# Kernel tuning notes

Measured on AMD Instinct MI355X. Metric: run time of the kernel, lower is better.

Reference implementation:

```python
import jax, jax.numpy as jnp
import numpy as np

LN_EPS = 1e-5


def setup_inputs() -> dict:
    key = jax.random.key(0)
    k0, k1, k2, k3 = jax.random.split(key, 4)
    b, X, Y, w1, w2, d = 16, 16, 16, 8, 8, 128
    heads = 4
    x = jax.random.normal(k0, (b, X, Y, w1, w2, d), dtype=jnp.float32)
    gamma = jnp.ones((d,), dtype=jnp.float32)
    beta = jnp.zeros((d,), dtype=jnp.float32)
    w_qkv = jax.random.normal(k1, (d, 3 * d), dtype=jnp.float32) * 0.02
    w_out = jax.random.normal(k2, (d, d), dtype=jnp.float32) * 0.02
    bias_table = jax.random.normal(k3, ((2 * w1 - 1) * (2 * w2 - 1), heads), dtype=jnp.float32) * 0.02
    return {"x": x, "gamma": gamma, "beta": beta, "w_qkv": w_qkv,
            "w_out": w_out, "bias_table": bias_table,
            "window_height": 8, "window_width": 8}


def _rel_pos_indices(wh, ww):
    gh = jnp.arange(wh)
    gw = jnp.arange(ww)
    grid = jnp.stack(jnp.meshgrid(gh, gw, indexing='ij'), axis=-1).reshape(-1, 2)  # [n, 2]
    rel = grid[:, None, :] - grid[None, :, :]  # [n, n, 2]
    rel = rel + jnp.array([wh - 1, ww - 1])
    return rel[..., 0] * (2 * ww - 1) + rel[..., 1]  # [n, n]


def reference(x, gamma, beta, w_qkv, w_out, bias_table, window_height, window_width):
    b, X, Y, w1, w2, d = x.shape
    heads = bias_table.shape[-1]
    dh = d // heads
    scale = dh ** -0.5

    # LayerNorm over channel dim
    mu = x.mean(axis=-1, keepdims=True)
    var = jnp.mean((x - mu) ** 2, axis=-1, keepdims=True)
    xn = (x - mu) * jax.lax.rsqrt(var + LN_EPS) * gamma + beta

    n = w1 * w2
    xn = xn.reshape(b * X * Y, n, d)  # [B, n, d], B = b*X*Y windows

    qkv = xn @ w_qkv  # [B, n, 3d]
    q, k, v = jnp.split(qkv, 3, axis=-1)
    def split_heads(t):
        return t.reshape(t.shape[0], n, heads, dh).transpose(0, 2, 1, 3)  # [B, h, n, dh]
    q, k, v = map(split_heads, (q, k, v))

    sim = jnp.einsum('bhid,bhjd->bhij', q * scale, k)  # [B, h, n, n]

    idx = _rel_pos_indices(window_height, window_width)  # [n, n]
    bias = bias_table[idx].transpose(2, 0, 1)  # [h, n, n]

    attn = jax.nn.softmax(sim + bias, axis=-1)
    out = jnp.einsum('bhij,bhjd->bhid', attn, v)  # [B, h, n, dh]
    out = out.transpose(0, 2, 1, 3).reshape(b * X * Y, w1, w2, d)
    out = out @ w_out
    return out.reshape(b, X, Y, w1, w2, d)
```

## Files before the change

### kernel.cpp

```cpp
#include <hip/hip_runtime.h>

typedef __attribute__((ext_vector_type(4))) short short4v;
typedef __attribute__((ext_vector_type(8))) short short8;
typedef __attribute__((ext_vector_type(4))) float f32x4;

#define NWIN 4096

__device__ __forceinline__ short f2bf(float f) {
    unsigned int u = __builtin_bit_cast(unsigned int, f);
    u += 0x7fffu + ((u >> 16) & 1u);
    return (short)(u >> 16);
}

__device__ __forceinline__ unsigned pack2h(float a, float b) {
    unsigned ua = __builtin_bit_cast(unsigned, a) + 0x8000u;
    unsigned ub = __builtin_bit_cast(unsigned, b) + 0x8000u;
    return (ua >> 16) | (ub & 0xffff0000u);
}

__device__ __forceinline__ short4v pk4h(float a, float b, float c, float d) {
    uint2 u;
    u.x = pack2h(a, b);
    u.y = pack2h(c, d);
    return __builtin_bit_cast(short4v, u);
}

#define LOG2E 1.4426950408889634f
#define QSCALE 0.17677669529663687f

__global__ void prep_kernel(const float* __restrict__ w_qkv,
                            const float* __restrict__ w_out,
                            const float* __restrict__ bias_table,
                            short* __restrict__ wqkvT,
                            short* __restrict__ woutT,
                            float* __restrict__ biasP)
{
    int id = blockIdx.x * 256 + threadIdx.x;
    if (id < 49152) {
        int j = id >> 7, k = id & 127;
        float v = w_qkv[k * 384 + j];
        if (j < 128) v *= (QSCALE * LOG2E);
        wqkvT[id] = f2bf(v);
    } else if (id < 65536) {
        int t = id - 49152;
        int j = t >> 7, k = t & 127;
        woutT[t] = f2bf(w_out[k * 128 + j]);
    } else if (id < 81920) {
        int t = id - 65536;
        int m  = t & 15;
        int ln = (t >> 4) & 63;
        int ib = (t >> 10) & 3;
        int h  = t >> 12;
        int lo = ln & 15, g = ln >> 4;
        int i = ib * 16 + lo;
        int j = (m >> 2) * 16 + g * 4 + (m & 3);
        int ri = i >> 3, ci = i & 7, rj = j >> 3, cj = j & 7;
        int idx = (ri - rj + 7) * 15 + (ci - cj + 7);
        biasP[t] = bias_table[idx * 4 + h] * LOG2E;
    }
}

__global__ __launch_bounds__(256, 3)
void attn_kernel(const float* __restrict__ x,
                 const float* __restrict__ gamma,
                 const float* __restrict__ beta,
                 const short* __restrict__ wqkvT,
                 const short* __restrict__ woutT,
                 const float* __restrict__ biasP,
                 float* __restrict__ out)
{
    __shared__ __align__(16) char smem[32768];

    const int tid = threadIdx.x;
    const int h  = tid >> 6;
    const int ln = tid & 63;
    const int lo = ln & 15, g = ln >> 4;

    const float* xwin = x + (size_t)blockIdx.x * 8192;

    float4 va[4][2];
    #pragma unroll
    for (int p = 0; p < 4; ++p) {
        int t = h * 16 + p * 4 + g;
        const float4* xr = (const float4*)(xwin + t * 128 + lo * 8);
        va[p][0] = xr[0];
        va[p][1] = xr[1];
    }

    short8 pwk[2];
    #pragma unroll
    for (int cb = 0; cb < 2; ++cb)
        pwk[cb] = *(const short8*)(wqkvT + (128 + h * 32 + cb * 16 + lo) * 128 + g * 8);

    float4 ga0 = ((const float4*)gamma)[lo * 2], ga1 = ((const float4*)gamma)[lo * 2 + 1];
    float4 be0 = ((const float4*)beta)[lo * 2],  be1 = ((const float4*)beta)[lo * 2 + 1];

    #pragma unroll
    for (int p = 0; p < 4; ++p) {
        int t = h * 16 + p * 4 + g;
        float4 v0 = va[p][0], v1 = va[p][1];
        float s  = v0.x + v0.y + v0.z + v0.w + v1.x + v1.y + v1.z + v1.w;
        float sq = v0.x*v0.x + v0.y*v0.y + v0.z*v0.z + v0.w*v0.w
                 + v1.x*v1.x + v1.y*v1.y + v1.z*v1.z + v1.w*v1.w;
        #pragma unroll
        for (int m = 1; m < 16; m <<= 1) {
            s  += __shfl_xor(s, m, 64);
            sq += __shfl_xor(sq, m, 64);
        }
        float mu  = s * (1.f / 128.f);
        float var = sq * (1.f / 128.f) - mu * mu;
        float rs  = rsqrtf(var + 1e-5f);
        float y0 = (v0.x - mu) * rs * ga0.x + be0.x;
        float y1 = (v0.y - mu) * rs * ga0.y + be0.y;
        float y2 = (v0.z - mu) * rs * ga0.z + be0.z;
        float y3 = (v0.w - mu) * rs * ga0.w + be0.w;
        float y4 = (v1.x - mu) * rs * ga1.x + be1.x;
        float y5 = (v1.y - mu) * rs * ga1.y + be1.y;
        float y6 = (v1.z - mu) * rs * ga1.z + be1.z;
        float y7 = (v1.w - mu) * rs * ga1.w + be1.w;
        uint4 pk;
        pk.x = pack2h(y0, y1); pk.y = pack2h(y2, y3);
        pk.z = pack2h(y4, y5); pk.w = pack2h(y6, y7);
        *(uint4*)(smem + ((t * 256 + lo * 16) ^ ((t & 7) << 4))) = pk;
    }
    __syncthreads();

    const f32x4 z4 = {0.f, 0.f, 0.f, 0.f};

    short4v kA[2][4], qB[2][4], vA[2][4];
    {
        f32x4 acc[2][4];
        #pragma unroll
        for (int a = 0; a < 2; ++a)
            #pragma unroll
            for (int b = 0; b < 4; ++b) acc[a][b] = z4;
        #pragma unroll
        for (int kk = 0; kk < 4; ++kk) {
            short8 xa[4];
            #pragma unroll
            for (int tb = 0; tb < 4; ++tb) {
                int t = tb * 16 + lo;
                xa[tb] = *(const short8*)(smem + ((t * 256 + kk * 64 + g * 16) ^ ((t & 7) << 4)));
            }
            #pragma unroll
            for (int cb = 0; cb < 2; ++cb) {
                short8 wkf = (kk == 0) ? pwk[cb]
                    : *(const short8*)(wqkvT + (128 + h * 32 + cb * 16 + lo) * 128 + kk * 32 + g * 8);
                #pragma unroll
                for (int tb = 0; tb < 4; ++tb)
                    acc[cb][tb] = __builtin_amdgcn_mfma_f32_16x16x32_bf16(wkf, xa[tb], acc[cb][tb], 0, 0, 0);
            }
        }
        #pragma unroll
        for (int ck = 0; ck < 2; ++ck)
            #pragma unroll
            for (int tb = 0; tb < 4; ++tb)
                kA[ck][tb] = pk4h(acc[ck][tb][0], acc[ck][tb][1], acc[ck][tb][2], acc[ck][tb][3]);
    }
    {
        f32x4 acc[2][4];
        #pragma unroll
        for (int a = 0; a < 2; ++a)
            #pragma unroll
            for (int b = 0; b < 4; ++b) acc[a][b] = z4;
        #pragma unroll
        for (int kk = 0; kk < 4; ++kk) {
            short8 xa[4];
            #pragma unroll
            for (int tb = 0; tb < 4; ++tb) {
                int t = tb * 16 + lo;
                xa[tb] = *(const short8*)(smem + ((t * 256 + kk * 64 + g * 16) ^ ((t & 7) << 4)));
            }
            #pragma unroll
            for (int cb = 0; cb < 2; ++cb) {
                short8 wqf = *(const short8*)(wqkvT + (h * 32 + cb * 16 + lo) * 128 + kk * 32 + g * 8);
                #pragma unroll
                for (int tb = 0; tb < 4; ++tb)
                    acc[cb][tb] = __builtin_amdgcn_mfma_f32_16x16x32_bf16(wqf, xa[tb], acc[cb][tb], 0, 0, 0);
            }
        }
        #pragma unroll
        for (int ck = 0; ck < 2; ++ck)
            #pragma unroll
            for (int tb = 0; tb < 4; ++tb)
                qB[ck][tb] = pk4h(acc[ck][tb][0], acc[ck][tb][1], acc[ck][tb][2], acc[ck][tb][3]);
    }
    {
        f32x4 acc[4][2];
        #pragma unroll
        for (int a = 0; a < 4; ++a)
            #pragma unroll
            for (int b = 0; b < 2; ++b) acc[a][b] = z4;
        #pragma unroll
        for (int kk = 0; kk < 4; ++kk) {
            short8 xa[4];
            #pragma unroll
            for (int tb = 0; tb < 4; ++tb) {
                int t = tb * 16 + lo;
                xa[tb] = *(const short8*)(smem + ((t * 256 + kk * 64 + g * 16) ^ ((t & 7) << 4)));
            }
            #pragma unroll
            for (int cb = 0; cb < 2; ++cb) {
                short8 wvf = *(const short8*)(wqkvT + (256 + h * 32 + cb * 16 + lo) * 128 + kk * 32 + g * 8);
                #pragma unroll
                for (int tb = 0; tb < 4; ++tb)
                    acc[tb][cb] = __builtin_amdgcn_mfma_f32_16x16x32_bf16(xa[tb], wvf, acc[tb][cb], 0, 0, 0);
            }
        }
        #pragma unroll
        for (int cb = 0; cb < 2; ++cb)
            #pragma unroll
            for (int jk = 0; jk < 4; ++jk)
                vA[cb][jk] = pk4h(acc[jk][cb][0], acc[jk][cb][1], acc[jk][cb][2], acc[jk][cb][3]);
    }

    f32x4 ot[2][4];
    #pragma unroll
    for (int a = 0; a < 2; ++a)
        #pragma unroll
        for (int b = 0; b < 4; ++b) ot[a][b] = z4;

    float inv[4];
    #pragma unroll
    for (int ib = 0; ib < 4; ++ib) {
        const f32x4* bp = (const f32x4*)(biasP + ((h * 4 + ib) * 64 + ln) * 16);
        f32x4 st[4];
        #pragma unroll
        for (int jb = 0; jb < 4; ++jb) st[jb] = bp[jb];
        __builtin_amdgcn_s_setprio(1);
        #pragma unroll
        for (int jb = 0; jb < 4; ++jb) {
            st[jb] = __builtin_amdgcn_mfma_f32_16x16x16bf16_1k(kA[0][jb], qB[0][ib], st[jb], 0, 0, 0);
            st[jb] = __builtin_amdgcn_mfma_f32_16x16x16bf16_1k(kA[1][jb], qB[1][ib], st[jb], 0, 0, 0);
        }
        __builtin_amdgcn_s_setprio(0);

        float s = 0.f;
        short4v pB[4];
        #pragma unroll
        for (int jb = 0; jb < 4; ++jb) {
            float e0 = __builtin_exp2f(st[jb][0]);
            float e1 = __builtin_exp2f(st[jb][1]);
            float e2 = __builtin_exp2f(st[jb][2]);
            float e3 = __builtin_exp2f(st[jb][3]);
            s += (e0 + e1) + (e2 + e3);
            pB[jb] = pk4h(e0, e1, e2, e3);
        }
        s += __shfl_xor(s, 16, 64);
        s += __shfl_xor(s, 32, 64);
        inv[ib] = 1.f / s;

        __builtin_amdgcn_s_setprio(1);
        #pragma unroll
        for (int jk = 0; jk < 4; ++jk)
            #pragma unroll
            for (int cb = 0; cb < 2; ++cb)
                ot[cb][ib] = __builtin_amdgcn_mfma_f32_16x16x16bf16_1k(vA[cb][jk], pB[jk], ot[cb][ib], 0, 0, 0);
        __builtin_amdgcn_s_setprio(0);
    }

    char* aob = smem + 16384;
    #pragma unroll
    for (int cb = 0; cb < 2; ++cb)
        #pragma unroll
        for (int ib = 0; ib < 4; ++ib) {
            int i = ib * 16 + lo;
            float sc = inv[ib];
            uint2 w;
            w.x = pack2h(ot[cb][ib][0] * sc, ot[cb][ib][1] * sc);
            w.y = pack2h(ot[cb][ib][2] * sc, ot[cb][ib][3] * sc);
            *(uint2*)(aob + ((i * 256 + (h * 32 + cb * 16 + g * 4) * 2) ^ ((i & 7) << 4))) = w;
        }

    short8 wof_c[2];
    #pragma unroll
    for (int cj = 0; cj < 2; ++cj)
        wof_c[cj] = *(const short8*)(woutT + (h * 32 + cj * 16 + lo) * 128 + g * 8);

    __syncthreads();

    f32x4 ft[2][4];
    #pragma unroll
    for (int a = 0; a < 2; ++a)
        #pragma unroll
        for (int b = 0; b < 4; ++b) ft[a][b] = z4;

    short8 ao_c[4];
    #pragma unroll
    for (int tb = 0; tb < 4; ++tb) {
        int t = tb * 16 + lo;
        ao_c[tb] = *(const short8*)(aob + ((t * 256 + g * 16) ^ ((t & 7) << 4)));
    }

    #pragma unroll
    for (int kk = 0; kk < 4; ++kk) {
        short8 ao_n[4], wof_n[2];
        if (kk < 3) {
            #pragma unroll
            for (int tb = 0; tb < 4; ++tb) {
                int t = tb * 16 + lo;
                ao_n[tb] = *(const short8*)(aob + ((t * 256 + (kk + 1) * 64 + g * 16) ^ ((t & 7) << 4)));
            }
            #pragma unroll
            for (int cj = 0; cj < 2; ++cj)
                wof_n[cj] = *(const short8*)(woutT + (h * 32 + cj * 16 + lo) * 128 + (kk + 1) * 32 + g * 8);
        }
        __builtin_amdgcn_s_setprio(1);
        #pragma unroll
        for (int cj = 0; cj < 2; ++cj)
            #pragma unroll
            for (int tb = 0; tb < 4; ++tb)
                ft[cj][tb] = __builtin_amdgcn_mfma_f32_16x16x32_bf16(wof_c[cj], ao_c[tb], ft[cj][tb], 0, 0, 0);
        __builtin_amdgcn_s_setprio(0);
        if (kk < 3) {
            #pragma unroll
            for (int tb = 0; tb < 4; ++tb) ao_c[tb] = ao_n[tb];
            wof_c[0] = wof_n[0];
            wof_c[1] = wof_n[1];
        }
    }

    float* owin = out + (size_t)blockIdx.x * 8192;
    #pragma unroll
    for (int cj = 0; cj < 2; ++cj)
        #pragma unroll
        for (int tb = 0; tb < 4; ++tb) {
            int t = tb * 16 + lo;
            *(f32x4*)(owin + t * 128 + h * 32 + cj * 16 + g * 4) = ft[cj][tb];
        }
}

extern "C" void kernel_launch(void* const* d_in, const int* in_sizes, int n_in,
                              void* d_out, int out_size, void* d_ws, size_t ws_size,
                              hipStream_t stream) {
    const float* x          = (const float*)d_in[0];
    const float* gamma      = (const float*)d_in[1];
    const float* beta       = (const float*)d_in[2];
    const float* w_qkv      = (const float*)d_in[3];
    const float* w_out      = (const float*)d_in[4];
    const float* bias_table = (const float*)d_in[5];

    short* wqkvT = (short*)d_ws;
    short* woutT = (short*)((char*)d_ws + 98304);
    float* biasP = (float*)((char*)d_ws + 131072);

    prep_kernel<<<320, 256, 0, stream>>>(w_qkv, w_out, bias_table, wqkvT, woutT, biasP);
    attn_kernel<<<NWIN, 256, 0, stream>>>(x, gamma, beta, wqkvT, woutT, biasP, (float*)d_out);
}
```

Measured before the change: 114.0 us.

## Process two windows per block to reuse weight fragments and interleave MFMAs

Each block now handles two attention windows instead of one, halving the grid. Every weight fragment and bias load is shared across both windows, and the MFMA chains for the two windows are interleaved to give more independent instructions. It doubles shared memory to 64KB, lowers the launch-bounds occupancy target from 3 to 2, and raises register pressure, which may cost latency hiding.

```diff
diff --git a/kernel.cpp b/kernel.cpp
--- a/kernel.cpp
+++ b/kernel.cpp
@@ -60,7 +60,7 @@
     }
 }
 
-__global__ __launch_bounds__(256, 3)
+__global__ __launch_bounds__(256, 2)
 void attn_kernel(const float* __restrict__ x,
                  const float* __restrict__ gamma,
                  const float* __restrict__ beta,
@@ -69,22 +69,24 @@
                  const float* __restrict__ biasP,
                  float* __restrict__ out)
 {
-    __shared__ __align__(16) char smem[32768];
+    __shared__ __align__(16) char smem[65536];
 
     const int tid = threadIdx.x;
     const int h  = tid >> 6;
     const int ln = tid & 63;
     const int lo = ln & 15, g = ln >> 4;
 
-    const float* xwin = x + (size_t)blockIdx.x * 8192;
-
-    float4 va[4][2];
+    const float* xw0 = x + (size_t)(2 * blockIdx.x) * 8192;
+    const float* xw1 = xw0 + 8192;
+
+    float4 va[2][4][2];
     #pragma unroll
     for (int p = 0; p < 4; ++p) {
         int t = h * 16 + p * 4 + g;
-        const float4* xr = (const float4*)(xwin + t * 128 + lo * 8);
-        va[p][0] = xr[0];
-        va[p][1] = xr[1];
+        const float4* xr0 = (const float4*)(xw0 + t * 128 + lo * 8);
+        const float4* xr1 = (const float4*)(xw1 + t * 128 + lo * 8);
+        va[0][p][0] = xr0[0]; va[0][p][1] = xr0[1];
+        va[1][p][0] = xr1[0]; va[1][p][1] = xr1[1];
     }
 
     short8 pwk[2];
@@ -96,237 +98,272 @@
     float4 be0 = ((const float4*)beta)[lo * 2],  be1 = ((const float4*)beta)[lo * 2 + 1];
 
     #pragma unroll
-    for (int p = 0; p < 4; ++p) {
-        int t = h * 16 + p * 4 + g;
-        float4 v0 = va[p][0], v1 = va[p][1];
-        float s  = v0.x + v0.y + v0.z + v0.w + v1.x + v1.y + v1.z + v1.w;
-        float sq = v0.x*v0.x + v0.y*v0.y + v0.z*v0.z + v0.w*v0.w
-                 + v1.x*v1.x + v1.y*v1.y + v1.z*v1.z + v1.w*v1.w;
-        #pragma unroll
-        for (int m = 1; m < 16; m <<= 1) {
-            s  += __shfl_xor(s, m, 64);
-            sq += __shfl_xor(sq, m, 64);
-        }
-        float mu  = s * (1.f / 128.f);
-        float var = sq * (1.f / 128.f) - mu * mu;
-        float rs  = rsqrtf(var + 1e-5f);
-        float y0 = (v0.x - mu) * rs * ga0.x + be0.x;
-        float y1 = (v0.y - mu) * rs * ga0.y + be0.y;
-        float y2 = (v0.z - mu) * rs * ga0.z + be0.z;
-        float y3 = (v0.w - mu) * rs * ga0.w + be0.w;
-        float y4 = (v1.x - mu) * rs * ga1.x + be1.x;
-        float y5 = (v1.y - mu) * rs * ga1.y + be1.y;
-        float y6 = (v1.z - mu) * rs * ga1.z + be1.z;
-        float y7 = (v1.w - mu) * rs * ga1.w + be1.w;
-        uint4 pk;
-        pk.x = pack2h(y0, y1); pk.y = pack2h(y2, y3);
-        pk.z = pack2h(y4, y5); pk.w = pack2h(y6, y7);
-        *(uint4*)(smem + ((t * 256 + lo * 16) ^ ((t & 7) << 4))) = pk;
+    for (int w = 0; w < 2; ++w) {
+        #pragma unroll
+        for (int p = 0; p < 4; ++p) {
+            int t = h * 16 + p * 4 + g;
+            float4 v0 = va[w][p][0], v1 = va[w][p][1];
+            float s  = v0.x + v0.y + v0.z + v0.w + v1.x + v1.y + v1.z + v1.w;
+            float sq = v0.x*v0.x + v0.y*v0.y + v0.z*v0.z + v0.w*v0.w
+                     + v1.x*v1.x + v1.y*v1.y + v1.z*v1.z + v1.w*v1.w;
+            #pragma unroll
+            for (int m = 1; m < 16; m <<= 1) {
+                s  += __shfl_xor(s, m, 64);
+                sq += __shfl_xor(sq, m, 64);
+            }
+            float mu  = s * (1.f / 128.f);
+            float var = sq * (1.f / 128.f) - mu * mu;
+            float rs  = rsqrtf(var + 1e-5f);
+            float y0 = (v0.x - mu) * rs * ga0.x + be0.x;
+            float y1 = (v0.y - mu) * rs * ga0.y + be0.y;
+            float y2 = (v0.z - mu) * rs * ga0.z + be0.z;
+            float y3 = (v0.w - mu) * rs * ga0.w + be0.w;
+            float y4 = (v1.x - mu) * rs * ga1.x + be1.x;
+            float y5 = (v1.y - mu) * rs * ga1.y + be1.y;
+            float y6 = (v1.z - mu) * rs * ga1.z + be1.z;
+            float y7 = (v1.w - mu) * rs * ga1.w + be1.w;
+            uint4 pk;
+            pk.x = pack2h(y0, y1); pk.y = pack2h(y2, y3);
+            pk.z = pack2h(y4, y5); pk.w = pack2h(y6, y7);
+            *(uint4*)(smem + w * 16384 + ((t * 256 + lo * 16) ^ ((t & 7) << 4))) = pk;
+        }
     }
     __syncthreads();
 
     const f32x4 z4 = {0.f, 0.f, 0.f, 0.f};
 
-    short4v kA[2][4], qB[2][4], vA[2][4];
+    short4v kA[2][2][4], qB[2][2][4], vA[2][2][4];
+
     {
-        f32x4 acc[2][4];
-        #pragma unroll
-        for (int a = 0; a < 2; ++a)
-            #pragma unroll
-            for (int b = 0; b < 4; ++b) acc[a][b] = z4;
+        f32x4 acc[2][2][4];
+        #pragma unroll
+        for (int w = 0; w < 2; ++w)
+            #pragma unroll
+            for (int a = 0; a < 2; ++a)
+                #pragma unroll
+                for (int b = 0; b < 4; ++b) acc[w][a][b] = z4;
         #pragma unroll
         for (int kk = 0; kk < 4; ++kk) {
-            short8 xa[4];
-            #pragma unroll
-            for (int tb = 0; tb < 4; ++tb) {
-                int t = tb * 16 + lo;
-                xa[tb] = *(const short8*)(smem + ((t * 256 + kk * 64 + g * 16) ^ ((t & 7) << 4)));
-            }
+            short8 xa[2][4];
+            #pragma unroll
+            for (int w = 0; w < 2; ++w)
+                #pragma unroll
+                for (int tb = 0; tb < 4; ++tb) {
+                    int t = tb * 16 + lo;
+                    xa[w][tb] = *(const short8*)(smem + w * 16384 +
+                        ((t * 256 + kk * 64 + g * 16) ^ ((t & 7) << 4)));
+                }
             #pragma unroll
             for (int cb = 0; cb < 2; ++cb) {
                 short8 wkf = (kk == 0) ? pwk[cb]
                     : *(const short8*)(wqkvT + (128 + h * 32 + cb * 16 + lo) * 128 + kk * 32 + g * 8);
                 #pragma unroll
+                for (int tb = 0; tb < 4; ++tb) {
+                    acc[0][cb][tb] = __builtin_amdgcn_mfma_f32_16x16x32_bf16(wkf, xa[0][tb], acc[0][cb][tb], 0, 0, 0);
+                    acc[1][cb][tb] = __builtin_amdgcn_mfma_f32_16x16x32_bf16(wkf, xa[1][tb], acc[1][cb][tb], 0, 0, 0);
+                }
+            }
+        }
+        #pragma unroll
+        for (int w = 0; w < 2; ++w)
+            #pragma unroll
+            for (int ck = 0; ck < 2; ++ck)
+                #pragma unroll
                 for (int tb = 0; tb < 4; ++tb)
-                    acc[cb][tb] = __builtin_amdgcn_mfma_f32_16x16x32_bf16(wkf, xa[tb], acc[cb][tb], 0, 0, 0);
-            }
-        }
-        #pragma unroll
-        for (int ck = 0; ck < 2; ++ck)
-            #pragma unroll
-            for (int tb = 0; tb < 4; ++tb)
-                kA[ck][tb] = pk4h(acc[ck][tb][0], acc[ck][tb][1], acc[ck][tb][2], acc[ck][tb][3]);
+                    kA[w][ck][tb] = pk4h(acc[w][ck][tb][0], acc[w][ck][tb][1], acc[w][ck][tb][2], acc[w][ck][tb][3]);
     }
     {
-        f32x4 acc[2][4];
+        f32x4 acc[2][2][4];
+        #pragma unroll
+        for (int w = 0; w < 2; ++w)
+            #pragma unroll
+            for (int a = 0; a < 2; ++a)
+                #pragma unroll
+                for (int b = 0; b < 4; ++b) acc[w][a][b] = z4;
+        #pragma unroll
+        for (int kk = 0; kk < 4; ++kk) {
+            short8 xa[2][4];
+            #pragma unroll
+            for (int w = 0; w < 2; ++w)
+                #pragma unroll
+                for (int tb = 0; tb < 4; ++tb) {
+                    int t = tb * 16 + lo;
+                    xa[w][tb] = *(const short8*)(smem + w * 16384 +
+                        ((t * 256 + kk * 64 + g * 16) ^ ((t & 7) << 4)));
+                }
+            #pragma unroll
+            for (int cb = 0; cb < 2; ++cb) {
+                short8 wqf = *(const short8*)(wqkvT + (h * 32 + cb * 16 + lo) * 128 + kk * 32 + g * 8);
+                #pragma unroll
+                for (int tb = 0; tb < 4; ++tb) {
+                    acc[0][cb][tb] = __builtin_amdgcn_mfma_f32_16x16x32_bf16(wqf, xa[0][tb], acc[0][cb][tb], 0, 0, 0);
+                    acc[1][cb][tb] = __builtin_amdgcn_mfma_f32_16x16x32_bf16(wqf, xa[1][tb], acc[1][cb][tb], 0, 0, 0);
+                }
+            }
+        }
+        #pragma unroll
+        for (int w = 0; w < 2; ++w)
+            #pragma unroll
+            for (int ck = 0; ck < 2; ++ck)
+                #pragma unroll
+                for (int tb = 0; tb < 4; ++tb)
+                    qB[w][ck][tb] = pk4h(acc[w][ck][tb][0], acc[w][ck][tb][1], acc[w][ck][tb][2], acc[w][ck][tb][3]);
+    }
+    {
+        f32x4 acc[2][4][2];
+        #pragma unroll
+        for (int w = 0; w < 2; ++w)
+            #pragma unroll
+            for (int a = 0; a < 4; ++a)
+                #pragma unroll
+                for (int b = 0; b < 2; ++b) acc[w][a][b] = z4;
+        #pragma unroll
+        for (int kk = 0; kk < 4; ++kk) {
+            short8 xa[2][4];
+            #pragma unroll
+            for (int w = 0; w < 2; ++w)
+                #pragma unroll
+                for (int tb = 0; tb < 4; ++tb) {
+                    int t = tb * 16 + lo;
+                    xa[w][tb] = *(const short8*)(smem + w * 16384 +
+                        ((t * 256 + kk * 64 + g * 16) ^ ((t & 7) << 4)));
+                }
+            #pragma unroll
+            for (int cb = 0; cb < 2; ++cb) {
+                short8 wvf = *(const short8*)(wqkvT + (256 + h * 32 + cb * 16 + lo) * 128 + kk * 32 + g * 8);
+                #pragma unroll
+                for (int tb = 0; tb < 4; ++tb) {
+                    acc[0][tb][cb] = __builtin_amdgcn_mfma_f32_16x16x32_bf16(xa[0][tb], wvf, acc[0][tb][cb], 0, 0, 0);
+                    acc[1][tb][cb] = __builtin_amdgcn_mfma_f32_16x16x32_bf16(xa[1][tb], wvf, acc[1][tb][cb], 0, 0, 0);
+                }
+            }
+        }
+        #pragma unroll
+        for (int w = 0; w < 2; ++w)
+            #pragma unroll
+            for (int cb = 0; cb < 2; ++cb)
+                #pragma unroll
+                for (int jk = 0; jk < 4; ++jk)
+                    vA[w][cb][jk] = pk4h(acc[w][jk][cb][0], acc[w][jk][cb][1], acc[w][jk][cb][2], acc[w][jk][cb][3]);
+    }
+
+    char* ao0 = smem + 32768;
+    char* ao1 = smem + 49152;
+    #pragma unroll
+    for (int ib = 0; ib < 4; ++ib) {
+        const f32x4* bp = (const f32x4*)(biasP + ((h * 4 + ib) * 64 + ln) * 16);
+        f32x4 stA[4], stB[4];
+        #pragma unroll
+        for (int jb = 0; jb < 4; ++jb) { f32x4 b = bp[jb]; stA[jb] = b; stB[jb] = b; }
+
+        __builtin_amdgcn_s_setprio(1);
+        #pragma unroll
+        for (int jb = 0; jb < 4; ++jb) {
+            stA[jb] = __builtin_amdgcn_mfma_f32_16x16x16bf16_1k(kA[0][0][jb], qB[0][0][ib], stA[jb], 0, 0, 0);
+            stB[jb] = __builtin_amdgcn_mfma_f32_16x16x16bf16_1k(kA[1][0][jb], qB[1][0][ib], stB[jb], 0, 0, 0);
+            stA[jb] = __builtin_amdgcn_mfma_f32_16x16x16bf16_1k(kA[0][1][jb], qB[0][1][ib], stA[jb], 0, 0, 0);
+            stB[jb] = __builtin_amdgcn_mfma_f32_16x16x16bf16_1k(kA[1][1][jb], qB[1][1][ib], stB[jb], 0, 0, 0);
+        }
+        __builtin_amdgcn_s_setprio(0);
+
+        float sA = 0.f, sB = 0.f;
+        short4v pA[4], pBv[4];
+        #pragma unroll
+        for (int jb = 0; jb < 4; ++jb) {
+            float a0 = __builtin_exp2f(stA[jb][0]);
+            float b0 = __builtin_exp2f(stB[jb][0]);
+            float a1 = __builtin_exp2f(stA[jb][1]);
+            float b1 = __builtin_exp2f(stB[jb][1]);
+            float a2 = __builtin_exp2f(stA[jb][2]);
+            float b2 = __builtin_exp2f(stB[jb][2]);
+            float a3 = __builtin_exp2f(stA[jb][3]);
+            float b3 = __builtin_exp2f(stB[jb][3]);
+            sA += (a0 + a1) + (a2 + a3);
+            sB += (b0 + b1) + (b2 + b3);
+            pA[jb]  = pk4h(a0, a1, a2, a3);
+            pBv[jb] = pk4h(b0, b1, b2, b3);
+        }
+        sA += __shfl_xor(sA, 16, 64);
+        sB += __shfl_xor(sB, 16, 64);
+        sA += __shfl_xor(sA, 32, 64);
+        sB += __shfl_xor(sB, 32, 64);
+        float invA = 1.f / sA, invB = 1.f / sB;
+
+        f32x4 otA[2] = {z4, z4}, otB[2] = {z4, z4};
+        __builtin_amdgcn_s_setprio(1);
+        #pragma unroll
+        for (int jk = 0; jk < 4; ++jk)
+            #pragma unroll
+            for (int cb = 0; cb < 2; ++cb) {
+                otA[cb] = __builtin_amdgcn_mfma_f32_16x16x16bf16_1k(vA[0][cb][jk], pA[jk],  otA[cb], 0, 0, 0);
+                otB[cb] = __builtin_amdgcn_mfma_f32_16x16x16bf16_1k(vA[1][cb][jk], pBv[jk], otB[cb], 0, 0, 0);
+            }
+        __builtin_amdgcn_s_setprio(0);
+
+        int i = ib * 16 + lo;
+        int sw = (i & 7) << 4;
+        #pragma unroll
+        for (int cb = 0; cb < 2; ++cb) {
+            uint2 wv0, wv1;
+            wv0.x = pack2h(otA[cb][0] * invA, otA[cb][1] * invA);
+            wv0.y = pack2h(otA[cb][2] * invA, otA[cb][3] * invA);
+            wv1.x = pack2h(otB[cb][0] * invB, otB[cb][1] * invB);
+            wv1.y = pack2h(otB[cb][2] * invB, otB[cb][3] * invB);
+            int byte = (i * 256 + (h * 32 + cb * 16 + g * 4) * 2) ^ sw;
+            *(uint2*)(ao0 + byte) = wv0;
+            *(uint2*)(ao1 + byte) = wv1;
+        }
+    }
+
+    short8 wof0[2];
+    #pragma unroll
+    for (int cj = 0; cj < 2; ++cj)
+        wof0[cj] = *(const short8*)(woutT + (h * 32 + cj * 16 + lo) * 128 + g * 8);
+
+    __syncthreads();
+
+    f32x4 ft[2][2][4];
+    #pragma unroll
+    for (int w = 0; w < 2; ++w)
         #pragma unroll
         for (int a = 0; a < 2; ++a)
             #pragma unroll
-            for (int b = 0; b < 4; ++b) acc[a][b] = z4;
-        #pragma unroll
-        for (int kk = 0; kk < 4; ++kk) {
-            short8 xa[4];
+            for (int b = 0; b < 4; ++b) ft[w][a][b] = z4;
+
+    #pragma unroll
+    for (int kk = 0; kk < 4; ++kk) {
+        short8 ao[2][4];
+        #pragma unroll
+        for (int w = 0; w < 2; ++w)
             #pragma unroll
             for (int tb = 0; tb < 4; ++tb) {
                 int t = tb * 16 + lo;
-                xa[tb] = *(const short8*)(smem + ((t * 256 + kk * 64 + g * 16) ^ ((t & 7) << 4)));
-            }
-            #pragma unroll
-            for (int cb = 0; cb < 2; ++cb) {
-                short8 wqf = *(const short8*)(wqkvT + (h * 32 + cb * 16 + lo) * 128 + kk * 32 + g * 8);
-                #pragma unroll
-                for (int tb = 0; tb < 4; ++tb)
-                    acc[cb][tb] = __builtin_amdgcn_mfma_f32_16x16x32_bf16(wqf, xa[tb], acc[cb][tb], 0, 0, 0);
-            }
-        }
-        #pragma unroll
-        for (int ck = 0; ck < 2; ++ck)
-            #pragma unroll
-            for (int tb = 0; tb < 4; ++tb)
-                qB[ck][tb] = pk4h(acc[ck][tb][0], acc[ck][tb][1], acc[ck][tb][2], acc[ck][tb][3]);
-    }
-    {
-        f32x4 acc[4][2];
-        #pragma unroll
-        for (int a = 0; a < 4; ++a)
-            #pragma unroll
-            for (int b = 0; b < 2; ++b) acc[a][b] = z4;
-        #pragma unroll
-        for (int kk = 0; kk < 4; ++kk) {
-            short8 xa[4];
+                ao[w][tb] = *(const short8*)((w ? ao1 : ao0) +
+                    ((t * 256 + kk * 64 + g * 16) ^ ((t & 7) << 4)));
+            }
+        __builtin_amdgcn_s_setprio(1);
+        #pragma unroll
+        for (int cj = 0; cj < 2; ++cj) {
+            short8 wof = (kk == 0) ? wof0[cj]
+                : *(const short8*)(woutT + (h * 32 + cj * 16 + lo) * 128 + kk * 32 + g * 8);
             #pragma unroll
             for (int tb = 0; tb < 4; ++tb) {
-                int t = tb * 16 + lo;
-                xa[tb] = *(const short8*)(smem + ((t * 256 + kk * 64 + g * 16) ^ ((t & 7) << 4)));
-            }
-            #pragma unroll
-            for (int cb = 0; cb < 2; ++cb) {
-                short8 wvf = *(const short8*)(wqkvT + (256 + h * 32 + cb * 16 + lo) * 128 + kk * 32 + g * 8);
-                #pragma unroll
-                for (int tb = 0; tb < 4; ++tb)
-                    acc[tb][cb] = __builtin_amdgcn_mfma_f32_16x16x32_bf16(xa[tb], wvf, acc[tb][cb], 0, 0, 0);
-            }
-        }
-        #pragma unroll
-        for (int cb = 0; cb < 2; ++cb)
-            #pragma unroll
-            for (int jk = 0; jk < 4; ++jk)
-                vA[cb][jk] = pk4h(acc[jk][cb][0], acc[jk][cb][1], acc[jk][cb][2], acc[jk][cb][3]);
-    }
-
-    f32x4 ot[2][4];
-    #pragma unroll
-    for (int a = 0; a < 2; ++a)
-        #pragma unroll
-        for (int b = 0; b < 4; ++b) ot[a][b] = z4;
-
-    float inv[4];
-    #pragma unroll
-    for (int ib = 0; ib < 4; ++ib) {
-        const f32x4* bp = (const f32x4*)(biasP + ((h * 4 + ib) * 64 + ln) * 16);
-        f32x4 st[4];
-        #pragma unroll
-        for (int jb = 0; jb < 4; ++jb) st[jb] = bp[jb];
-        __builtin_amdgcn_s_setprio(1);
-        #pragma unroll
-        for (int jb = 0; jb < 4; ++jb) {
-            st[jb] = __builtin_amdgcn_mfma_f32_16x16x16bf16_1k(kA[0][jb], qB[0][ib], st[jb], 0, 0, 0);
-            st[jb] = __builtin_amdgcn_mfma_f32_16x16x16bf16_1k(kA[1][jb], qB[1][ib], st[jb], 0, 0, 0);
+                ft[0][cj][tb] = __builtin_amdgcn_mfma_f32_16x16x32_bf16(wof, ao[0][tb], ft[0][cj][tb], 0, 0, 0);
+                ft[1][cj][tb] = __builtin_amdgcn_mfma_f32_16x16x32_bf16(wof, ao[1][tb], ft[1][cj][tb], 0, 0, 0);
+            }
         }
         __builtin_amdgcn_s_setprio(0);
-
-        float s = 0.f;
-        short4v pB[4];
-        #pragma unroll
-        for (int jb = 0; jb < 4; ++jb) {
-            float e0 = __builtin_exp2f(st[jb][0]);
-            float e1 = __builtin_exp2f(st[jb][1]);
-            float e2 = __builtin_exp2f(st[jb][2]);
-            float e3 = __builtin_exp2f(st[jb][3]);
-            s += (e0 + e1) + (e2 + e3);
-            pB[jb] = pk4h(e0, e1, e2, e3);
-        }
-        s += __shfl_xor(s, 16, 64);
-        s += __shfl_xor(s, 32, 64);
-        inv[ib] = 1.f / s;
-
-        __builtin_amdgcn_s_setprio(1);
-        #pragma unroll
-        for (int jk = 0; jk < 4; ++jk)
-            #pragma unroll
-            for (int cb = 0; cb < 2; ++cb)
-                ot[cb][ib] = __builtin_amdgcn_mfma_f32_16x16x16bf16_1k(vA[cb][jk], pB[jk], ot[cb][ib], 0, 0, 0);
-        __builtin_amdgcn_s_setprio(0);
-    }
-
-    char* aob = smem + 16384;
-    #pragma unroll
-    for (int cb = 0; cb < 2; ++cb)
-        #pragma unroll
-        for (int ib = 0; ib < 4; ++ib) {
-            int i = ib * 16 + lo;
-            float sc = inv[ib];
-            uint2 w;
-            w.x = pack2h(ot[cb][ib][0] * sc, ot[cb][ib][1] * sc);
-            w.y = pack2h(ot[cb][ib][2] * sc, ot[cb][ib][3] * sc);
-            *(uint2*)(aob + ((i * 256 + (h * 32 + cb * 16 + g * 4) * 2) ^ ((i & 7) << 4))) = w;
-        }
-
-    short8 wof_c[2];
-    #pragma unroll
-    for (int cj = 0; cj < 2; ++cj)
-        wof_c[cj] = *(const short8*)(woutT + (h * 32 + cj * 16 + lo) * 128 + g * 8);
-
-    __syncthreads();
-
-    f32x4 ft[2][4];
-    #pragma unroll
-    for (int a = 0; a < 2; ++a)
-        #pragma unroll
-        for (int b = 0; b < 4; ++b) ft[a][b] = z4;
-
-    short8 ao_c[4];
-    #pragma unroll
-    for (int tb = 0; tb < 4; ++tb) {
-        int t = tb * 16 + lo;
-        ao_c[tb] = *(const short8*)(aob + ((t * 256 + g * 16) ^ ((t & 7) << 4)));
-    }
-
-    #pragma unroll
-    for (int kk = 0; kk < 4; ++kk) {
-        short8 ao_n[4], wof_n[2];
-        if (kk < 3) {
-            #pragma unroll
-            for (int tb = 0; tb < 4; ++tb) {
-                int t = tb * 16 + lo;
-                ao_n[tb] = *(const short8*)(aob + ((t * 256 + (kk + 1) * 64 + g * 16) ^ ((t & 7) << 4)));
-            }
-            #pragma unroll
-            for (int cj = 0; cj < 2; ++cj)
-                wof_n[cj] = *(const short8*)(woutT + (h * 32 + cj * 16 + lo) * 128 + (kk + 1) * 32 + g * 8);
-        }
-        __builtin_amdgcn_s_setprio(1);
-        #pragma unroll
-        for (int cj = 0; cj < 2; ++cj)
-            #pragma unroll
-            for (int tb = 0; tb < 4; ++tb)
-                ft[cj][tb] = __builtin_amdgcn_mfma_f32_16x16x32_bf16(wof_c[cj], ao_c[tb], ft[cj][tb], 0, 0, 0);
-        __builtin_amdgcn_s_setprio(0);
-        if (kk < 3) {
-            #pragma unroll
-            for (int tb = 0; tb < 4; ++tb) ao_c[tb] = ao_n[tb];
-            wof_c[0] = wof_n[0];
-            wof_c[1] = wof_n[1];
-        }
-    }
-
-    float* owin = out + (size_t)blockIdx.x * 8192;
+    }
+
+    float* ow0 = out + (size_t)(2 * blockIdx.x) * 8192;
+    float* ow1 = ow0 + 8192;
     #pragma unroll
     for (int cj = 0; cj < 2; ++cj)
         #pragma unroll
         for (int tb = 0; tb < 4; ++tb) {
             int t = tb * 16 + lo;
-            *(f32x4*)(owin + t * 128 + h * 32 + cj * 16 + g * 4) = ft[cj][tb];
+            *(f32x4*)(ow0 + t * 128 + h * 32 + cj * 16 + g * 4) = ft[0][cj][tb];
+            *(f32x4*)(ow1 + t * 128 + h * 32 + cj * 16 + g * 4) = ft[1][cj][tb];
         }
 }
 
@@ -345,5 +382,5 @@
     float* biasP = (float*)((char*)d_ws + 131072);
 
     prep_kernel<<<320, 256, 0, stream>>>(w_qkv, w_out, bias_table, wqkvT, woutT, biasP);
-    attn_kernel<<<NWIN, 256, 0, stream>>>(x, gamma, beta, wqkvT, woutT, biasP, (float*)d_out);
-}
+    attn_kernel<<<NWIN / 2, 256, 0, stream>>>(x, gamma, beta, wqkvT, woutT, biasP, (float*)d_out);
+}
```

Measured after the change: 149.7 us. 1.31x slower.
